# Performance work log

Hardware: AMD Instinct MI355X
Metric: run time of the kernel (lower is better)

The kernel has to match this reference:

```python
import jax, jax.numpy as jnp
import numpy as np

NUM_HEADS = 16
CAUSAL = True


def setup_inputs() -> dict:
    key = jax.random.key(0)
    ks = jax.random.split(key, 3)
    B, T, D = 2, 2048, 1024
    s = 1.0 / np.sqrt(D)
    return {
        "x": jax.random.normal(ks[0], (B, T, D), dtype=jnp.float32),
        "W_qkv": jax.random.normal(ks[1], (3 * D, D), dtype=jnp.float32) * s,
        "b_qkv": jnp.zeros((3 * D,), dtype=jnp.float32),
        "W_out": jax.random.normal(ks[2], (D, D), dtype=jnp.float32) * s,
        "b_out": jnp.zeros((D,), dtype=jnp.float32),
    }


def reference(x, W_qkv, b_qkv, W_out, b_out):
    B, T, D = x.shape
    H = NUM_HEADS
    hd = D // H
    # qkv projection: torch Linear y = x @ W.T + b
    qkv = jnp.einsum('btd,ed->bte', x, W_qkv) + b_qkv  # [B,T,3D]
    qkv = qkv.reshape(B, T, H, 3 * hd).transpose(0, 2, 1, 3)  # [B,H,T,3hd]
    q, k, v = jnp.split(qkv, 3, axis=-1)  # each [B,H,T,hd]
    scale = 1.0 / np.sqrt(hd).astype(np.float32)
    scores = jnp.einsum('bhtd,bhsd->bhts', q, k) * scale  # [B,H,T,T]
    if CAUSAL:
        mask = jnp.triu(jnp.ones((T, T), dtype=bool), k=1)
        scores = jnp.where(mask, jnp.float32(-jnp.inf), scores)
    weights = jax.nn.softmax(scores, axis=-1)
    attn = jnp.einsum('bhts,bhsd->bhtd', weights, v)  # [B,H,T,hd]
    out = attn.transpose(0, 2, 1, 3).reshape(B, T, D)
    return jnp.einsum('btd,ed->bte', out, W_out) + b_out
```

## Files before the change

### kernel.cpp

```cpp
#include <hip/hip_runtime.h>
#include <hip/hip_bf16.h>
#include <cstdint>


using short8  = __attribute__((ext_vector_type(8))) short;
using floatx4 = __attribute__((ext_vector_type(4))) float;

#define LDS_STRIDE 40

__device__ __forceinline__ float bf16_to_f32(unsigned short u) {
    union { unsigned int i; float f; } v; v.i = ((unsigned int)u) << 16; return v.f;
}
__device__ __forceinline__ unsigned short f32_to_bf16(float f) {
    union { float f; unsigned int i; } v; v.f = f;
    unsigned int x = v.i;
    unsigned int r = x + 0x7FFFu + ((x >> 16) & 1u);
    return (unsigned short)(r >> 16);
}
__device__ __forceinline__ short8 cvt8(const float* __restrict__ p) {
    const float4 f0 = *(const float4*)p;
    const float4 f1 = *(const float4*)(p + 4);
    short8 r;
    r[0] = (short)f32_to_bf16(f0.x); r[1] = (short)f32_to_bf16(f0.y);
    r[2] = (short)f32_to_bf16(f0.z); r[3] = (short)f32_to_bf16(f0.w);
    r[4] = (short)f32_to_bf16(f1.x); r[5] = (short)f32_to_bf16(f1.y);
    r[6] = (short)f32_to_bf16(f1.z); r[7] = (short)f32_to_bf16(f1.w);
    return r;
}
__device__ __forceinline__ unsigned int cvtpk(float a, float b) {
    unsigned int r;
    asm("v_cvt_pk_bf16_f32 %0, %1, %2" : "=v"(r) : "v"(a), "v"(b));
    return r;
}

#define Q_PRESCALE 0.1803368801111204f

#if __has_builtin(__builtin_amdgcn_global_load_lds)
#define ASYNC_STAGE 1
typedef const __attribute__((address_space(1))) void* gas1_t;
typedef __attribute__((address_space(3))) void* las3_t;
#else
#define ASYNC_STAGE 0
#endif

__device__ __forceinline__ void gload_lds16(const ushort* g, ushort* l) {
#if ASYNC_STAGE
    __builtin_amdgcn_global_load_lds((gas1_t)g, (las3_t)l, 16, 0, 0);
#else
    *(short8*)l = *(const short8*)g;
#endif
}

__device__ __forceinline__ int v_slot(int k) {
    const int k5 = k & 31;
    return (k & 32) + ((k5 >> 4) & 1) * 4 + ((k5 >> 2) & 3) * 8 + (k5 & 3);
}

__global__ __launch_bounds__(256, 8) void cvt_bf16_3(
    const float* __restrict__ x,  const float* __restrict__ wq,
    const float* __restrict__ wo, ushort* __restrict__ xb,
    ushort* __restrict__ wqb, ushort* __restrict__ wob)
{
    const int i = blockIdx.x * 256 + threadIdx.x;
    const float* src; ushort* dst; int off;
    if (i < 524288)      { src = x;  dst = xb;  off = i; }
    else if (i < 917504) { src = wq; dst = wqb; off = i - 524288; }
    else                 { src = wo; dst = wob; off = i - 917504; }
    *(short8*)(dst + (size_t)off * 8) = cvt8(src + (size_t)off * 8);
}

template <int MODE>
__global__ __launch_bounds__(256, 3) void gemm_bf16(
    const ushort* __restrict__ A, const ushort* __restrict__ W,
    const float* __restrict__ bias,
    ushort* __restrict__ Cq, ushort* __restrict__ Ck, ushort* __restrict__ Cv,
    float* __restrict__ Cout, int M, int N, int K)
{
    __shared__ __align__(16) ushort As[2][128 * 32];
    __shared__ __align__(16) ushort Bs[2][128 * 32];

    const int tid  = threadIdx.x;
    const int lane = tid & 63;
    const int wave = tid >> 6;
    const int wm = (wave >> 1) * 64;
    const int wn = (wave & 1) * 64;
    const int m0 = blockIdx.x * 128;
    const int n0 = blockIdx.y * 128;
    const int quad = lane >> 4;
    const int l16  = lane & 15;

    floatx4 acc[4][4];
#pragma unroll
    for (int i = 0; i < 4; i++)
#pragma unroll
        for (int j = 0; j < 4; j++) acc[i][j] = (floatx4)0.0f;

    const int ob0 = tid * 16, ob1 = ob0 + 4096;
    const int ln0 = ob0 >> 7, p0_ = ((ob0 >> 4) & 7) ^ (ln0 & 7);
    const int ln1 = ob1 >> 7, p1_ = ((ob1 >> 4) & 7) ^ (ln1 & 7);
    const int row0 = ln0 * 2 + (p0_ >> 2), ch0 = p0_ & 3;
    const int row1 = ln1 * 2 + (p1_ >> 2), ch1 = p1_ & 3;
    const ushort* pA0 = A + (size_t)(m0 + row0) * K + ch0 * 8;
    const ushort* pA1 = A + (size_t)(m0 + row1) * K + ch1 * 8;
    const ushort* pB0 = W + (size_t)(n0 + row0) * K + ch0 * 8;
    const ushort* pB1 = W + (size_t)(n0 + row1) * K + ch1 * 8;

    const int Ra = wm + l16;
    const int aoff = (Ra >> 1) * 64 + (((((Ra & 1) << 2) + quad) ^ ((Ra >> 1) & 7)) << 3);
    const int Rb = wn + l16;
    const int boff = (Rb >> 1) * 64 + (((((Rb & 1) << 2) + quad) ^ ((Rb >> 1) & 7)) << 3);

    auto stage = [&](int k0, ushort* AsB, ushort* BsB) {
        gload_lds16(pA0 + k0, AsB + wave * 512);
        gload_lds16(pA1 + k0, AsB + 2048 + wave * 512);
        gload_lds16(pB0 + k0, BsB + wave * 512);
        gload_lds16(pB1 + k0, BsB + 2048 + wave * 512);
    };
    auto compute = [&](const ushort* AsB, const ushort* BsB) {
        short8 af[4], bf[4];
#pragma unroll
        for (int i = 0; i < 4; i++)
            af[i] = *(const short8*)&AsB[aoff + i * 512];
#pragma unroll
        for (int j = 0; j < 4; j++)
            bf[j] = *(const short8*)&BsB[boff + j * 512];
#pragma unroll
        for (int i = 0; i < 4; i++)
#pragma unroll
            for (int j = 0; j < 4; j++)
                acc[i][j] = __builtin_amdgcn_mfma_f32_16x16x32_bf16(af[i], bf[j], acc[i][j], 0, 0, 0);
    };

#if ASYNC_STAGE
    stage(0, As[0], Bs[0]);
    __syncthreads();
    int k = 0;
    while (true) {
        if (k + 32 < K) stage(k + 32, As[1], Bs[1]);
        compute(As[0], Bs[0]);
        __syncthreads();
        k += 32; if (k >= K) break;
        if (k + 32 < K) stage(k + 32, As[0], Bs[0]);
        compute(As[1], Bs[1]);
        __syncthreads();
        k += 32; if (k >= K) break;
    }
#else
    for (int k0 = 0; k0 < K; k0 += 32) {
        const short8 a0 = *(const short8*)(pA0 + k0);
        const short8 a1 = *(const short8*)(pA1 + k0);
        const short8 b0 = *(const short8*)(pB0 + k0);
        const short8 b1 = *(const short8*)(pB1 + k0);
        __syncthreads();
        *(short8*)((char*)As[0] + ob0) = a0;
        *(short8*)((char*)As[0] + ob1) = a1;
        *(short8*)((char*)Bs[0] + ob0) = b0;
        *(short8*)((char*)Bs[0] + ob1) = b1;
        __syncthreads();
        compute(As[0], Bs[0]);
    }
#endif

#pragma unroll
    for (int i = 0; i < 4; i++) {
#pragma unroll
        for (int j = 0; j < 4; j++) {
#pragma unroll
            for (int r = 0; r < 4; r++) {
                const int row = m0 + wm + i * 16 + quad * 4 + r;
                const int col = n0 + wn + j * 16 + l16;
                float v = acc[i][j][r] + bias[col];
                if (MODE == 0) {
                    const int h  = col / 192;
                    const int rr = col - h * 192;
                    const int sel = rr >> 6;
                    const int d   = rr & 63;
                    const int b = row >> 11;
                    const int t = row & 2047;
                    const int bh = b * 16 + h;
                    if (sel == 0) {
                        Cq[(((size_t)bh) * 2048 + t) * 64 + d] =
                            f32_to_bf16(v * Q_PRESCALE);
                    } else if (sel == 1) {
                        Ck[(((size_t)bh) * 2048 + t) * 64 + d] = f32_to_bf16(v);
                    } else {
                        Cv[(((size_t)bh * 32 + (t >> 6)) * 64 + d) * 64 + v_slot(t & 63)] =
                            f32_to_bf16(v);
                    }
                } else {
                    Cout[(size_t)row * N + col] = v;
                }
            }
        }
    }
}

template <int MODE, int AFP32>
__global__ __launch_bounds__(256, 2) void gemm_bt(
    const void* __restrict__ Av, const float* __restrict__ W,
    const float* __restrict__ bias,
    ushort* __restrict__ Cq, ushort* __restrict__ Ck, ushort* __restrict__ Cv,
    float* __restrict__ Cout, int M, int N, int K)
{
    __shared__ __align__(16) ushort As[128 * LDS_STRIDE];
    __shared__ __align__(16) ushort Bs[128 * LDS_STRIDE];

    const int tid  = threadIdx.x;
    const int lane = tid & 63;
    const int wave = tid >> 6;
    const int wm = (wave >> 1) * 64;
    const int wn = (wave & 1) * 64;
    const int m0 = blockIdx.x * 128;
    const int n0 = blockIdx.y * 128;
    const int quad = lane >> 4;
    const int l16  = lane & 15;

    floatx4 acc[4][4];
#pragma unroll
    for (int i = 0; i < 4; i++)
#pragma unroll
        for (int j = 0; j < 4; j++) acc[i][j] = (floatx4)0.0f;

    const int srow = tid >> 2;
    const int scol = (tid & 3) * 8;

    for (int k0 = 0; k0 < K; k0 += 32) {
        short8 a0, a1;
        if (AFP32) {
            const float* A = (const float*)Av;
            a0 = cvt8(A + (size_t)(m0 + srow) * K + k0 + scol);
            a1 = cvt8(A + (size_t)(m0 + srow + 64) * K + k0 + scol);
        } else {
            const ushort* A = (const ushort*)Av;
            a0 = *(const short8*)(A + (size_t)(m0 + srow) * K + k0 + scol);
            a1 = *(const short8*)(A + (size_t)(m0 + srow + 64) * K + k0 + scol);
        }
        const short8 b0 = cvt8(W + (size_t)(n0 + srow) * K + k0 + scol);
        const short8 b1 = cvt8(W + (size_t)(n0 + srow + 64) * K + k0 + scol);
        __syncthreads();
        *(short8*)&As[srow * LDS_STRIDE + scol] = a0;
        *(short8*)&As[(srow + 64) * LDS_STRIDE + scol] = a1;
        *(short8*)&Bs[srow * LDS_STRIDE + scol] = b0;
        *(short8*)&Bs[(srow + 64) * LDS_STRIDE + scol] = b1;
        __syncthreads();

        short8 af[4], bf[4];
#pragma unroll
        for (int i = 0; i < 4; i++)
            af[i] = *(const short8*)&As[(wm + i * 16 + l16) * LDS_STRIDE + quad * 8];
#pragma unroll
        for (int j = 0; j < 4; j++)
            bf[j] = *(const short8*)&Bs[(wn + j * 16 + l16) * LDS_STRIDE + quad * 8];
#pragma unroll
        for (int i = 0; i < 4; i++)
#pragma unroll
            for (int j = 0; j < 4; j++)
                acc[i][j] = __builtin_amdgcn_mfma_f32_16x16x32_bf16(af[i], bf[j], acc[i][j], 0, 0, 0);
    }

#pragma unroll
    for (int i = 0; i < 4; i++) {
#pragma unroll
        for (int j = 0; j < 4; j++) {
#pragma unroll
            for (int r = 0; r < 4; r++) {
                const int row = m0 + wm + i * 16 + quad * 4 + r;
                const int col = n0 + wn + j * 16 + l16;
                float v = acc[i][j][r] + bias[col];
                if (MODE == 0) {
                    const int h  = col / 192;
                    const int rr = col - h * 192;
                    const int sel = rr >> 6;
                    const int d   = rr & 63;
                    const int b = row >> 11;
                    const int t = row & 2047;
                    const int bh = b * 16 + h;
                    if (sel == 0) {
                        Cq[(((size_t)bh) * 2048 + t) * 64 + d] =
                            f32_to_bf16(v * Q_PRESCALE);
                    } else if (sel == 1) {
                        Ck[(((size_t)bh) * 2048 + t) * 64 + d] = f32_to_bf16(v);
                    } else {
                        Cv[(((size_t)bh * 32 + (t >> 6)) * 64 + d) * 64 + v_slot(t & 63)] =
                            f32_to_bf16(v);
                    }
                } else {
                    Cout[(size_t)row * N + col] = v;
                }
            }
        }
    }
}

__global__ __launch_bounds__(256, 4) void attn_mfma(
    const ushort* __restrict__ Q, const ushort* __restrict__ K,
    const ushort* __restrict__ Vtb, ushort* __restrict__ O)
{
    const int bid   = blockIdx.x;
    const int bh    = bid & 31;
    const int qtIdx = bid >> 5;
    const int qi    = (qtIdx < 16) ? (31 - qtIdx) : (qtIdx - 16);
    const int tid  = threadIdx.x;
    const int wave = tid >> 6;
    const int lane = tid & 63;
    const int quad = lane >> 4;
    const int l16  = lane & 15;
    const int qb   = qi * 64 + wave * 16;

    __shared__ __align__(16) ushort Ks[2][4096];
    __shared__ __align__(16) ushort Vs[2][4096];

    const size_t kbase = (size_t)bh * 2048 * 64;

    const int ob0 = tid * 16, ob1 = ob0 + 4096;
    const int r0 = ob0 >> 7, c0 = (ob0 >> 4) & 7;
    const int r1 = ob1 >> 7, c1 = (ob1 >> 4) & 7;
    const int e0 = r0 * 64 + ((c0 ^ (r0 & 7)) << 3);
    const int e1 = r1 * 64 + ((c1 ^ (r1 & 7)) << 3);
    const ushort* Kb = K + kbase;
    const ushort* Vb = Vtb + (size_t)bh * 32 * 4096;

    auto stage = [&](int t, ushort* KsB, ushort* VsB) {
        const ushort* Ktile = Kb + t * 4096;
        const ushort* Vtile = Vb + t * 4096;
        gload_lds16(Ktile + e0, KsB + wave * 512);
        gload_lds16(Ktile + e1, KsB + 2048 + wave * 512);
        gload_lds16(Vtile + e0, VsB + wave * 512);
        gload_lds16(Vtile + e1, VsB + 2048 + wave * 512);
    };

    const int sw0 = ((quad ^ (l16 & 7)) << 3);
    const int sw1 = (((4 + quad) ^ (l16 & 7)) << 3);
    const int rbase = l16 * 64;

    short8 qf0, qf1;
    {
        const ushort* qp = Q + kbase + (size_t)(qb + l16) * 64 + quad * 8;
        qf0 = *(const short8*)qp;
        qf1 = *(const short8*)(qp + 32);
    }

    floatx4 accO[4];
#pragma unroll
    for (int d = 0; d < 4; d++) accO[d] = (floatx4)0.0f;
    float accLs = 0.0f;

    union PB { unsigned int u[4]; short8 s8; };

    auto compute = [&](int t, const ushort* KsB, const ushort* VsB) {
        short8 kf[4][2];
#pragma unroll
        for (int j = 0; j < 4; j++) {
            kf[j][0] = *(const short8*)&KsB[j * 1024 + rbase + sw0];
            kf[j][1] = *(const short8*)&KsB[j * 1024 + rbase + sw1];
        }
        floatx4 sc[4];
#pragma unroll
        for (int j = 0; j < 4; j++) {
            floatx4 acc = (floatx4)0.0f;
            acc = __builtin_amdgcn_mfma_f32_16x16x32_bf16(kf[j][0], qf0, acc, 0, 0, 0);
            acc = __builtin_amdgcn_mfma_f32_16x16x32_bf16(kf[j][1], qf1, acc, 0, 0, 0);
            sc[j] = acc;
        }
        if (t * 64 + 63 > qb) {
            const int qcol = qb + l16;
#pragma unroll
            for (int j = 0; j < 4; j++) {
                const int keyb = t * 64 + j * 16 + quad * 4;
#pragma unroll
                for (int r = 0; r < 4; r++)
                    if (keyb + r > qcol) sc[j][r] = -1e30f;
            }
        }
#pragma unroll
        for (int j = 0; j < 4; j++)
#pragma unroll
            for (int r = 0; r < 4; r++)
                sc[j][r] = __builtin_amdgcn_exp2f(sc[j][r]);
        const floatx4 ssum = sc[0] + sc[1] + sc[2] + sc[3];
        accLs += (ssum[0] + ssum[1]) + (ssum[2] + ssum[3]);
        PB p0, p1;
#pragma unroll
        for (int j = 0; j < 2; j++) {
            p0.u[j * 2 + 0] = cvtpk(sc[j][0], sc[j][1]);
            p0.u[j * 2 + 1] = cvtpk(sc[j][2], sc[j][3]);
            p1.u[j * 2 + 0] = cvtpk(sc[j + 2][0], sc[j + 2][1]);
            p1.u[j * 2 + 1] = cvtpk(sc[j + 2][2], sc[j + 2][3]);
        }
        short8 vf[4][2];
#pragma unroll
        for (int d = 0; d < 4; d++) {
            vf[d][0] = *(const short8*)&VsB[d * 1024 + rbase + sw0];
            vf[d][1] = *(const short8*)&VsB[d * 1024 + rbase + sw1];
        }
#pragma unroll
        for (int d = 0; d < 4; d++) {
            accO[d] = __builtin_amdgcn_mfma_f32_16x16x32_bf16(p0.s8, vf[d][0], accO[d], 0, 0, 0);
            accO[d] = __builtin_amdgcn_mfma_f32_16x16x32_bf16(p1.s8, vf[d][1], accO[d], 0, 0, 0);
        }
    };

    const int nt = qi + 1;
    stage(0, Ks[0], Vs[0]);
    __syncthreads();
    int t = 0;
    while (true) {
        if (t + 1 < nt) stage(t + 1, Ks[1], Vs[1]);
        compute(t, Ks[0], Vs[0]);
        __syncthreads();
        if (++t >= nt) break;
        if (t + 1 < nt) stage(t + 1, Ks[0], Vs[0]);
        compute(t, Ks[1], Vs[1]);
        __syncthreads();
        if (++t >= nt) break;
    }

    const int b = bh >> 4, h = bh & 15;
    {
        float L = accLs;
        L += __shfl_xor(L, 16);
        L += __shfl_xor(L, 32);
        float inv[4];
#pragma unroll
        for (int r = 0; r < 4; r++) inv[r] = 1.0f / __shfl(L, quad * 4 + r);
#pragma unroll
        for (int d = 0; d < 4; d++)
#pragma unroll
            for (int r = 0; r < 4; r++)
                O[(size_t)(b * 2048 + qb + quad * 4 + r) * 1024 + h * 64 + d * 16 + l16] =
                    f32_to_bf16(accO[d][r] * inv[r]);
    }
}

extern "C" void kernel_launch(void* const* d_in, const int* in_sizes, int n_in,
                              void* d_out, int out_size, void* d_ws, size_t ws_size,
                              hipStream_t stream) {
    const float* x    = (const float*)d_in[0];
    const float* Wqkv = (const float*)d_in[1];
    const float* bqkv = (const float*)d_in[2];
    const float* Wout = (const float*)d_in[3];
    const float* bout = (const float*)d_in[4];
    float* out = (float*)d_out;

    char* ws = (char*)d_ws;
    const size_t MB = 1024 * 1024;
    ushort* Q    = (ushort*)(ws + 0 * MB);
    ushort* Kk   = (ushort*)(ws + 8 * MB);
    ushort* Vtb  = (ushort*)(ws + 16 * MB);
    ushort* O    = (ushort*)(ws + 24 * MB);

    const dim3 blk(256);
    if (ws_size >= 48 * MB) {
        ushort* xb    = (ushort*)(ws + 32 * MB);
        ushort* Wqkvb = (ushort*)(ws + 40 * MB);
        ushort* Woutb = (ushort*)(ws + 46 * MB);
        cvt_bf16_3<<<dim3(4096), blk, 0, stream>>>(x, Wqkv, Wout, xb, Wqkvb, Woutb);
        gemm_bf16<0><<<dim3(32, 24), blk, 0, stream>>>(xb, Wqkvb, bqkv, Q, Kk, Vtb,
                                                       nullptr, 4096, 3072, 1024);
        attn_mfma<<<dim3(1024), blk, 0, stream>>>(Q, Kk, Vtb, O);
        gemm_bf16<1><<<dim3(32, 8), blk, 0, stream>>>(O, Woutb, bout, nullptr, nullptr,
                                                      nullptr, out, 4096, 1024, 1024);
    } else {
        gemm_bt<0, 1><<<dim3(32, 24), blk, 0, stream>>>(x, Wqkv, bqkv, Q, Kk, Vtb,
                                                        nullptr, 4096, 3072, 1024);
        attn_mfma<<<dim3(1024), blk, 0, stream>>>(Q, Kk, Vtb, O);
        gemm_bt<1, 0><<<dim3(32, 8), blk, 0, stream>>>(O, Wout, bout, nullptr, nullptr,
                                                       nullptr, out, 4096, 1024, 1024);
    }
}
```

Baseline: 170.3 us.

## Deepen GEMM K-tile to 64 with single-buffered direct-to-LDS loads

Replaces the K=32 GEMM main loop (either double-buffered async or register-staged, chosen by a macro) with a single-buffered loop that stages a 128x64 K-slab per iteration using direct global-to-LDS loads. The LDS layout moves to one row per 64 elements with an XOR swizzle, and each iteration issues two MFMAs per accumulator, halving the number of loop iterations and barriers. The cost is that load and compute no longer overlap within a block, since both barriers wrap a single buffer. Latency hiding then relies on other resident blocks.

```diff
diff --git a/kernel.cpp b/kernel.cpp
--- a/kernel.cpp
+++ b/kernel.cpp
@@ -76,8 +76,8 @@
     ushort* __restrict__ Cq, ushort* __restrict__ Ck, ushort* __restrict__ Cv,
     float* __restrict__ Cout, int M, int N, int K)
 {
-    __shared__ __align__(16) ushort As[2][128 * 32];
-    __shared__ __align__(16) ushort Bs[2][128 * 32];
+    __shared__ __align__(16) ushort As[128 * 64];
+    __shared__ __align__(16) ushort Bs[128 * 64];
 
     const int tid  = threadIdx.x;
     const int lane = tid & 63;
@@ -95,71 +95,45 @@
 #pragma unroll
         for (int j = 0; j < 4; j++) acc[i][j] = (floatx4)0.0f;
 
-    const int ob0 = tid * 16, ob1 = ob0 + 4096;
-    const int ln0 = ob0 >> 7, p0_ = ((ob0 >> 4) & 7) ^ (ln0 & 7);
-    const int ln1 = ob1 >> 7, p1_ = ((ob1 >> 4) & 7) ^ (ln1 & 7);
-    const int row0 = ln0 * 2 + (p0_ >> 2), ch0 = p0_ & 3;
-    const int row1 = ln1 * 2 + (p1_ >> 2), ch1 = p1_ & 3;
-    const ushort* pA0 = A + (size_t)(m0 + row0) * K + ch0 * 8;
-    const ushort* pA1 = A + (size_t)(m0 + row1) * K + ch1 * 8;
-    const ushort* pB0 = W + (size_t)(n0 + row0) * K + ch0 * 8;
-    const ushort* pB1 = W + (size_t)(n0 + row1) * K + ch1 * 8;
+    const int rb  = tid >> 3;
+    const int lch = (tid & 7) ^ (rb & 7);
+    const ushort* pA = A + (size_t)(m0 + rb) * K + lch * 8;
+    const ushort* pB = W + (size_t)(n0 + rb) * K + lch * 8;
+    const size_t cstep = (size_t)32 * K;
 
     const int Ra = wm + l16;
-    const int aoff = (Ra >> 1) * 64 + (((((Ra & 1) << 2) + quad) ^ ((Ra >> 1) & 7)) << 3);
+    const int aoff0 = Ra * 64 + ((quad       ^ (Ra & 7)) << 3);
+    const int aoff1 = Ra * 64 + (((4 + quad) ^ (Ra & 7)) << 3);
     const int Rb = wn + l16;
-    const int boff = (Rb >> 1) * 64 + (((((Rb & 1) << 2) + quad) ^ ((Rb >> 1) & 7)) << 3);
-
-    auto stage = [&](int k0, ushort* AsB, ushort* BsB) {
-        gload_lds16(pA0 + k0, AsB + wave * 512);
-        gload_lds16(pA1 + k0, AsB + 2048 + wave * 512);
-        gload_lds16(pB0 + k0, BsB + wave * 512);
-        gload_lds16(pB1 + k0, BsB + 2048 + wave * 512);
-    };
-    auto compute = [&](const ushort* AsB, const ushort* BsB) {
-        short8 af[4], bf[4];
-#pragma unroll
-        for (int i = 0; i < 4; i++)
-            af[i] = *(const short8*)&AsB[aoff + i * 512];
-#pragma unroll
-        for (int j = 0; j < 4; j++)
-            bf[j] = *(const short8*)&BsB[boff + j * 512];
-#pragma unroll
-        for (int i = 0; i < 4; i++)
-#pragma unroll
-            for (int j = 0; j < 4; j++)
-                acc[i][j] = __builtin_amdgcn_mfma_f32_16x16x32_bf16(af[i], bf[j], acc[i][j], 0, 0, 0);
-    };
-
-#if ASYNC_STAGE
-    stage(0, As[0], Bs[0]);
-    __syncthreads();
-    int k = 0;
-    while (true) {
-        if (k + 32 < K) stage(k + 32, As[1], Bs[1]);
-        compute(As[0], Bs[0]);
-        __syncthreads();
-        k += 32; if (k >= K) break;
-        if (k + 32 < K) stage(k + 32, As[0], Bs[0]);
-        compute(As[1], Bs[1]);
-        __syncthreads();
-        k += 32; if (k >= K) break;
-    }
-#else
-    for (int k0 = 0; k0 < K; k0 += 32) {
-        const short8 a0 = *(const short8*)(pA0 + k0);
-        const short8 a1 = *(const short8*)(pA1 + k0);
-        const short8 b0 = *(const short8*)(pB0 + k0);
-        const short8 b1 = *(const short8*)(pB1 + k0);
-        __syncthreads();
-        *(short8*)((char*)As[0] + ob0) = a0;
-        *(short8*)((char*)As[0] + ob1) = a1;
-        *(short8*)((char*)Bs[0] + ob0) = b0;
-        *(short8*)((char*)Bs[0] + ob1) = b1;
-        __syncthreads();
-        compute(As[0], Bs[0]);
-    }
-#endif
+    const int boff0 = Rb * 64 + ((quad       ^ (Rb & 7)) << 3);
+    const int boff1 = Rb * 64 + (((4 + quad) ^ (Rb & 7)) << 3);
+
+    for (int k0 = 0; k0 < K; k0 += 64) {
+        __syncthreads();
+#pragma unroll
+        for (int c = 0; c < 4; c++) {
+            gload_lds16(pA + c * cstep + k0, &As[c * 2048 + wave * 512]);
+            gload_lds16(pB + c * cstep + k0, &Bs[c * 2048 + wave * 512]);
+        }
+        __syncthreads();
+
+        short8 af0[4], af1[4];
+#pragma unroll
+        for (int i = 0; i < 4; i++) {
+            af0[i] = *(const short8*)&As[aoff0 + i * 1024];
+            af1[i] = *(const short8*)&As[aoff1 + i * 1024];
+        }
+#pragma unroll
+        for (int j = 0; j < 4; j++) {
+            const short8 bf0 = *(const short8*)&Bs[boff0 + j * 1024];
+            const short8 bf1 = *(const short8*)&Bs[boff1 + j * 1024];
+#pragma unroll
+            for (int i = 0; i < 4; i++) {
+                acc[i][j] = __builtin_amdgcn_mfma_f32_16x16x32_bf16(af0[i], bf0, acc[i][j], 0, 0, 0);
+                acc[i][j] = __builtin_amdgcn_mfma_f32_16x16x32_bf16(af1[i], bf1, acc[i][j], 0, 0, 0);
+            }
+        }
+    }
 
 #pragma unroll
     for (int i = 0; i < 4; i++) {
```

Result: no change. 169.7 us (-0.4%).
